# Optimization experiments

Hardware: AMD Instinct MI355X
Metric: run time of the kernel (lower is better)

The kernel has to match this reference:

```python
import jax, jax.numpy as jnp
import numpy as np

N_U, N_P, E, E_LAB = 100000, 50000, 2000000, 500000
D_U, D_P, H = 64, 128, 64


def _seg_mean(feat, idx, n):
    # scatter-mean: sum per destination / clamp(count, 1)
    s = jax.ops.segment_sum(feat, idx, num_segments=n)
    c = jax.ops.segment_sum(jnp.ones((idx.shape[0],), feat.dtype), idx, num_segments=n)
    return s / jnp.maximum(c, 1.0)[:, None]


def setup_inputs() -> dict:
    key = jax.random.key(0)
    ks = jax.random.split(key, 16)
    inp = {
        'x_user': jax.random.normal(ks[0], (N_U, D_U), jnp.float32),
        'x_product': jax.random.normal(ks[1], (N_P, D_P), jnp.float32),
        'W1_buys_l': jax.random.normal(ks[2], (D_U, H), jnp.float32) * 0.05,
        'b1_buys': jnp.zeros((H,), jnp.float32),
        'W1_buys_r': jax.random.normal(ks[3], (D_P, H), jnp.float32) * 0.05,
        'W1_rev_l': jax.random.normal(ks[4], (D_P, H), jnp.float32) * 0.05,
        'b1_rev': jnp.zeros((H,), jnp.float32),
        'W1_rev_r': jax.random.normal(ks[5], (D_U, H), jnp.float32) * 0.05,
        'W2_buys_l': jax.random.normal(ks[6], (H, H), jnp.float32) * 0.05,
        'b2_buys': jnp.zeros((H,), jnp.float32),
        'W2_buys_r': jax.random.normal(ks[7], (H, H), jnp.float32) * 0.05,
        'W2_rev_l': jax.random.normal(ks[8], (H, H), jnp.float32) * 0.05,
        'b2_rev': jnp.zeros((H,), jnp.float32),
        'W2_rev_r': jax.random.normal(ks[9], (H, H), jnp.float32) * 0.05,
        'edge_src': jax.random.randint(ks[10], (E,), 0, N_U, jnp.int32),
        'edge_dst': jax.random.randint(ks[11], (E,), 0, N_P, jnp.int32),
        'lab_u': jax.random.randint(ks[12], (E_LAB,), 0, N_U, jnp.int32),
        'lab_p': jax.random.randint(ks[13], (E_LAB,), 0, N_P, jnp.int32),
    }
    return inp


def reference(x_user, x_product, W1_buys_l, b1_buys, W1_buys_r, W1_rev_l, b1_rev, W1_rev_r,
              W2_buys_l, b2_buys, W2_buys_r, W2_rev_l, b2_rev, W2_rev_r,
              edge_src, edge_dst, lab_u, lab_p):
    # SAGEConv (mean aggr): out_dst = mean_agg(x_src) @ W_l + b + x_dst @ W_r
    def sage(x_src, x_dst, src, dst, n_dst, Wl, b, Wr):
        agg = _seg_mean(x_src[src], dst, n_dst)
        return agg @ Wl + b + x_dst @ Wr

    n_u, n_p = x_user.shape[0], x_product.shape[0]
    # layer 1 (per edge type, hetero) + relu
    h_p = jax.nn.relu(sage(x_user, x_product, edge_src, edge_dst, n_p, W1_buys_l, b1_buys, W1_buys_r))
    h_u = jax.nn.relu(sage(x_product, x_user, edge_dst, edge_src, n_u, W1_rev_l, b1_rev, W1_rev_r))
    # layer 2
    h_p2 = sage(h_u, h_p, edge_src, edge_dst, n_p, W2_buys_l, b2_buys, W2_buys_r)
    h_u2 = sage(h_p, h_u, edge_dst, edge_src, n_u, W2_rev_l, b2_rev, W2_rev_r)
    # classifier: per-label-edge dot product
    return jnp.sum(h_u2[lab_u] * h_p2[lab_p], axis=-1)
```

## Files before the change

### kernel.cpp

```cpp
#include <hip/hip_runtime.h>


using u16 = unsigned short;
using u32 = unsigned int;

__device__ __forceinline__ u16 bf16r(float f) {
    u32 b = __float_as_uint(f);
    b += 0x7fffu + ((b >> 16) & 1u);
    return (u16)(b >> 16);
}
__device__ __forceinline__ float bflo(u32 u) { return __uint_as_float(u << 16); }
__device__ __forceinline__ float bfhi(u32 u) { return __uint_as_float(u & 0xffff0000u); }

#define BSH 8
#define MAXB 512
#define CHUNK 4096
#define RPT 16

__global__ __launch_bounds__(256) void k_histA(const int* __restrict__ esrc,
                                               const int* __restrict__ edst,
                                               int* __restrict__ bcntP,
                                               int* __restrict__ bcntU,
                                               int NBP, int NBU, int E) {
    __shared__ int hP[MAXB];
    __shared__ int hU[MAXB];
    int tid = threadIdx.x;
    for (int i = tid; i < MAXB; i += 256) { hP[i] = 0; hU[i] = 0; }
    __syncthreads();
    int E4 = E >> 2;
    const int4* s4 = (const int4*)esrc;
    const int4* d4 = (const int4*)edst;
    int stride = gridDim.x * 256;
    for (int i = blockIdx.x * 256 + tid; i < E4; i += stride) {
        int4 s = s4[i], d = d4[i];
        atomicAdd(&hU[s.x >> BSH], 1); atomicAdd(&hU[s.y >> BSH], 1);
        atomicAdd(&hU[s.z >> BSH], 1); atomicAdd(&hU[s.w >> BSH], 1);
        atomicAdd(&hP[d.x >> BSH], 1); atomicAdd(&hP[d.y >> BSH], 1);
        atomicAdd(&hP[d.z >> BSH], 1); atomicAdd(&hP[d.w >> BSH], 1);
    }
    if (blockIdx.x == 0 && tid < (E & 3)) {
        int e = E4 * 4 + tid;
        atomicAdd(&hU[esrc[e] >> BSH], 1);
        atomicAdd(&hP[edst[e] >> BSH], 1);
    }
    __syncthreads();
    for (int i = tid; i < NBP; i += 256) if (hP[i]) atomicAdd(&bcntP[i], hP[i]);
    for (int i = tid; i < NBU; i += 256) if (hU[i]) atomicAdd(&bcntU[i], hU[i]);
}

__global__ __launch_bounds__(256) void k_scanBuckets(const int* __restrict__ cntP,
                                                     int* __restrict__ basesP,
                                                     int* __restrict__ curP, int NBP,
                                                     const int* __restrict__ cntU,
                                                     int* __restrict__ basesU,
                                                     int* __restrict__ curU, int NBU) {
    const int* cnt; int* bases; int* cur; int NB;
    if (blockIdx.x == 0) { cnt = cntP; bases = basesP; cur = curP; NB = NBP; }
    else                 { cnt = cntU; bases = basesU; cur = curU; NB = NBU; }
    __shared__ int sA[MAXB];
    __shared__ int sB[MAXB];
    int tid = threadIdx.x;
    int v0 = (tid < NB) ? cnt[tid] : 0;
    int v1 = (tid + 256 < NB) ? cnt[tid + 256] : 0;
    sA[tid] = v0; sA[tid + 256] = v1;
    __syncthreads();
    int* src = sA; int* dst = sB;
    for (int off = 1; off < MAXB; off <<= 1) {
        dst[tid] = src[tid] + ((tid >= off) ? src[tid - off] : 0);
        int i2 = tid + 256;
        dst[i2] = src[i2] + ((i2 >= off) ? src[i2 - off] : 0);
        __syncthreads();
        int* t = src; src = dst; dst = t;
    }
    if (tid < NB)       { bases[tid] = src[tid] - v0;             cur[tid] = src[tid] - v0; }
    if (tid + 256 < NB) { bases[tid + 256] = src[tid + 256] - v1; cur[tid + 256] = src[tid + 256] - v1; }
    if (tid == 0) bases[NB] = src[MAXB - 1];
}

__global__ __launch_bounds__(256) void k_partition(const int* __restrict__ keys,
                                                   const int* __restrict__ payload,
                                                   int* __restrict__ cursor,
                                                   uint2* __restrict__ pairs,
                                                   int NB, int E) {
    __shared__ int hist[MAXB];
    __shared__ int sA[MAXB];
    __shared__ int sB[MAXB];
    __shared__ int bx[MAXB];
    __shared__ int gbase[MAXB];
    __shared__ uint2 prs[CHUNK];
    int tid = threadIdx.x;
    int i0 = blockIdx.x * CHUNK;
    int count = min(CHUNK, E - i0);
    for (int i = tid; i < MAXB; i += 256) hist[i] = 0;
    __syncthreads();
    int keyr[RPT], payr[RPT], rankr[RPT];
#pragma unroll
    for (int r = 0; r < RPT; ++r) {
        int idx = r * 256 + tid;
        if (idx < count) {
            int k = keys[i0 + idx];
            keyr[r] = k;
            payr[r] = payload[i0 + idx];
            rankr[r] = atomicAdd(&hist[k >> BSH], 1);
        } else keyr[r] = -1;
    }
    __syncthreads();
    sA[tid] = hist[tid]; sA[tid + 256] = hist[tid + 256];
    __syncthreads();
    int* src = sA; int* dst = sB;
    for (int off = 1; off < MAXB; off <<= 1) {
        dst[tid] = src[tid] + ((tid >= off) ? src[tid - off] : 0);
        int i2 = tid + 256;
        dst[i2] = src[i2] + ((i2 >= off) ? src[i2 - off] : 0);
        __syncthreads();
        int* t = src; src = dst; dst = t;
    }
    bx[tid] = src[tid] - hist[tid];
    bx[tid + 256] = src[tid + 256] - hist[tid + 256];
    __syncthreads();
    for (int b = tid; b < NB; b += 256) {
        int c = hist[b];
        gbase[b] = c ? atomicAdd(&cursor[b], c) : 0;
    }
#pragma unroll
    for (int r = 0; r < RPT; ++r) {
        if (keyr[r] >= 0)
            prs[bx[keyr[r] >> BSH] + rankr[r]] = make_uint2((u32)keyr[r], (u32)payr[r]);
    }
    __syncthreads();
    for (int j = tid; j < count; j += 256) {
        uint2 pr = prs[j];
        int b = pr.x >> BSH;
        pairs[gbase[b] + (j - bx[b])] = pr;
    }
}

__global__ __launch_bounds__(256) void k_bucketFill(
    const uint2* __restrict__ pairsP, const int* __restrict__ basesP, int NBP,
    int* __restrict__ nbr_p, int* __restrict__ deg_p, int* __restrict__ ptr_p, int NP,
    const uint2* __restrict__ pairsU, const int* __restrict__ basesU, int NBU,
    int* __restrict__ nbr_u, int* __restrict__ deg_u, int* __restrict__ ptr_u, int NU) {
    const uint2* pairs; const int* bases; int* nbr; int* deg; int* ptr; int N; int bucket;
    if ((int)blockIdx.x < NBP) {
        pairs = pairsP; bases = basesP; nbr = nbr_p; deg = deg_p; ptr = ptr_p; N = NP;
        bucket = blockIdx.x;
    } else {
        pairs = pairsU; bases = basesU; nbr = nbr_u; deg = deg_u; ptr = ptr_u; N = NU;
        bucket = blockIdx.x - NBP;
    }
    int tid = threadIdx.x;
    int base = bases[bucket];
    int cnt = bases[bucket + 1] - base;
    __shared__ int h[256];
    __shared__ int s[256];
    __shared__ int cur[256];
    h[tid] = 0;
    __syncthreads();
    for (int j = tid; j < cnt; j += 256) atomicAdd(&h[pairs[base + j].x & 255], 1);
    __syncthreads();
    int d = h[tid];
    s[tid] = d;
    __syncthreads();
    for (int off = 1; off < 256; off <<= 1) {
        int v = (tid >= off) ? s[tid - off] : 0;
        __syncthreads();
        s[tid] += v;
        __syncthreads();
    }
    int excl = s[tid] - d;
    int node = bucket * 256 + tid;
    if (node < N) { deg[node] = d; ptr[node] = base + excl; }
    cur[tid] = excl;
    __syncthreads();
    for (int j = tid; j < cnt; j += 256) {
        uint2 pr = pairs[base + j];
        int pos = atomicAdd(&cur[pr.x & 255], 1);
        nbr[base + pos] = pr.y;
    }
}

__global__ __launch_bounds__(256) void k_cast8(const float* __restrict__ x,
                                               u16* __restrict__ y, int n8) {
    int i = blockIdx.x * 256 + threadIdx.x;
    if (i >= n8) return;
    const float4* x4 = (const float4*)x;
    float4 a = x4[i * 2], b = x4[i * 2 + 1];
    uint4 o;
    o.x = (u32)bf16r(a.x) | ((u32)bf16r(a.y) << 16);
    o.y = (u32)bf16r(a.z) | ((u32)bf16r(a.w) << 16);
    o.z = (u32)bf16r(b.x) | ((u32)bf16r(b.y) << 16);
    o.w = (u32)bf16r(b.z) | ((u32)bf16r(b.w) << 16);
    ((uint4*)y)[i] = o;
}

__global__ __launch_bounds__(256) void k_gather1(const u16* __restrict__ y,
                                                 const int* __restrict__ nbr,
                                                 const int* __restrict__ stp,
                                                 const int* __restrict__ degp,
                                                 float* __restrict__ agg, int N) {
    int n = (blockIdx.x * 256 + threadIdx.x) >> 6;
    int lane = threadIdx.x & 63;
    if (n >= N) return;
    const int q = lane >> 3, t = lane & 7;
    const int d = degp[n];
    int j = stp[n];
    const int end = j + d;
    float a0=0,a1=0,a2=0,a3=0,a4=0,a5=0,a6=0,a7=0;
    float b0=0,b1=0,b2=0,b3=0,b4=0,b5=0,b6=0,b7=0;
    for (; j + 16 <= end; j += 16) {
        int g0 = nbr[j + q], g1 = nbr[j + 8 + q];
        uint4 v0 = *(const uint4*)(y + g0 * 64 + t * 8);
        uint4 v1 = *(const uint4*)(y + g1 * 64 + t * 8);
        a0 += bflo(v0.x); a1 += bfhi(v0.x); a2 += bflo(v0.y); a3 += bfhi(v0.y);
        a4 += bflo(v0.z); a5 += bfhi(v0.z); a6 += bflo(v0.w); a7 += bfhi(v0.w);
        b0 += bflo(v1.x); b1 += bfhi(v1.x); b2 += bflo(v1.y); b3 += bfhi(v1.y);
        b4 += bflo(v1.z); b5 += bfhi(v1.z); b6 += bflo(v1.w); b7 += bfhi(v1.w);
    }
    for (; j + 8 <= end; j += 8) {
        int g0 = nbr[j + q];
        uint4 v0 = *(const uint4*)(y + g0 * 64 + t * 8);
        a0 += bflo(v0.x); a1 += bfhi(v0.x); a2 += bflo(v0.y); a3 += bfhi(v0.y);
        a4 += bflo(v0.z); a5 += bfhi(v0.z); a6 += bflo(v0.w); a7 += bfhi(v0.w);
    }
    if (j + q < end) {
        int g0 = nbr[j + q];
        uint4 v0 = *(const uint4*)(y + g0 * 64 + t * 8);
        a0 += bflo(v0.x); a1 += bfhi(v0.x); a2 += bflo(v0.y); a3 += bfhi(v0.y);
        a4 += bflo(v0.z); a5 += bfhi(v0.z); a6 += bflo(v0.w); a7 += bfhi(v0.w);
    }
    a0 += b0; a1 += b1; a2 += b2; a3 += b3; a4 += b4; a5 += b5; a6 += b6; a7 += b7;
#pragma unroll
    for (int m = 8; m < 64; m <<= 1) {
        a0 += __shfl_xor(a0, m, 64); a1 += __shfl_xor(a1, m, 64);
        a2 += __shfl_xor(a2, m, 64); a3 += __shfl_xor(a3, m, 64);
        a4 += __shfl_xor(a4, m, 64); a5 += __shfl_xor(a5, m, 64);
        a6 += __shfl_xor(a6, m, 64); a7 += __shfl_xor(a7, m, 64);
    }
    if (q == 0) {
        float dinv = 1.0f / (float)max(d, 1);
        float* dstp = agg + n * 64 + t * 8;
        *(float4*)dstp       = make_float4(a0 * dinv, a1 * dinv, a2 * dinv, a3 * dinv);
        *(float4*)(dstp + 4) = make_float4(a4 * dinv, a5 * dinv, a6 * dinv, a7 * dinv);
    }
}

#define FMA_ROW(ACC, O, W4) \
    ACC[0] += (O) * (W4).x; ACC[1] += (O) * (W4).y; \
    ACC[2] += (O) * (W4).z; ACC[3] += (O) * (W4).w;

template <int K, int ROWS, bool RELU, bool EMIT, bool PRE, bool BIAS, bool STORE>
__global__ __launch_bounds__(256) void k_ctile(const float* __restrict__ pre,
                                               const float* __restrict__ bias,
                                               const float* __restrict__ x,
                                               const float* __restrict__ W,
                                               float* __restrict__ h,
                                               u16* __restrict__ hbf, int N) {
    constexpr int RR = ROWS / 16;
    constexpr int STRIDE = K + 4;
    constexpr int KF4 = K / 4;
    __shared__ float Ws[K * 64];
    __shared__ float op[ROWS * STRIDE];
    const int tid = threadIdx.x;
    for (int i = tid; i < K * 16; i += 256)
        ((float4*)Ws)[i] = ((const float4*)W)[i];
    const int c4 = (tid & 15) * 4;
    const int rb = (tid >> 4) * RR;
    float bx_ = 0.f, by_ = 0.f, bz_ = 0.f, bw_ = 0.f;
    if (BIAS) {
        float4 b4 = *(const float4*)(bias + c4);
        bx_ = b4.x; by_ = b4.y; bz_ = b4.z; bw_ = b4.w;
    }
    const int ntiles = (N + ROWS - 1) / ROWS;
    for (int tile = blockIdx.x; tile < ntiles; tile += gridDim.x) {
        const int row0 = tile * ROWS;
        __syncthreads();
        for (int i = tid; i < ROWS * KF4; i += 256) {
            int r = i / KF4, k4 = (i % KF4) * 4;
            int row = row0 + r;
            float4 v = make_float4(0.f, 0.f, 0.f, 0.f);
            if (row < N) v = *(const float4*)(x + (size_t)row * K + k4);
            *(float4*)(op + r * STRIDE + k4) = v;
        }
        __syncthreads();
        float acc[RR][4];
#pragma unroll
        for (int i = 0; i < RR; ++i) {
            float px = 0.f, py = 0.f, pz = 0.f, pw = 0.f;
            if (PRE) {
                int row = row0 + rb + i;
                if (row < N) {
                    float4 p = *(const float4*)(pre + row * 64 + c4);
                    px = p.x; py = p.y; pz = p.z; pw = p.w;
                }
            }
            acc[i][0] = bx_ + px; acc[i][1] = by_ + py;
            acc[i][2] = bz_ + pz; acc[i][3] = bw_ + pw;
        }
        for (int kk = 0; kk < K; kk += 4) {
            float4 w0 = *(const float4*)(Ws + (kk + 0) * 64 + c4);
            float4 w1 = *(const float4*)(Ws + (kk + 1) * 64 + c4);
            float4 w2 = *(const float4*)(Ws + (kk + 2) * 64 + c4);
            float4 w3 = *(const float4*)(Ws + (kk + 3) * 64 + c4);
#pragma unroll
            for (int i = 0; i < RR; ++i) {
                float4 o = *(const float4*)(op + (rb + i) * STRIDE + kk);
                FMA_ROW(acc[i], o.x, w0);
                FMA_ROW(acc[i], o.y, w1);
                FMA_ROW(acc[i], o.z, w2);
                FMA_ROW(acc[i], o.w, w3);
            }
        }
#pragma unroll
        for (int i = 0; i < RR; ++i) {
            int row = row0 + rb + i;
            if (row >= N) continue;
            float v0 = acc[i][0], v1 = acc[i][1], v2 = acc[i][2], v3 = acc[i][3];
            if (RELU) {
                v0 = fmaxf(v0, 0.f); v1 = fmaxf(v1, 0.f);
                v2 = fmaxf(v2, 0.f); v3 = fmaxf(v3, 0.f);
            }
            if (STORE)
                *(float4*)(h + row * 64 + c4) = make_float4(v0, v1, v2, v3);
            if (EMIT) {
                uint2 o;
                o.x = (u32)bf16r(v0) | ((u32)bf16r(v1) << 16);
                o.y = (u32)bf16r(v2) | ((u32)bf16r(v3) << 16);
                *(uint2*)(hbf + row * 64 + c4) = o;
            }
        }
    }
}

__global__ __launch_bounds__(256) void k_classify4(const float* __restrict__ hu,
                                                   const float* __restrict__ hp,
                                                   const int* __restrict__ lu,
                                                   const int* __restrict__ lp,
                                                   float* __restrict__ out, int EL) {
    int w = (blockIdx.x * 256 + threadIdx.x) >> 6;
    int lane = threadIdx.x & 63;
    int q = lane >> 4, t = lane & 15;
    int e = w * 4 + q;
    float v = 0.f;
    if (e < EL) {
        int u = lu[e], p = lp[e];
        float4 a = *(const float4*)(hu + u * 64 + t * 4);
        float4 b = *(const float4*)(hp + p * 64 + t * 4);
        v = a.x * b.x + a.y * b.y + a.z * b.z + a.w * b.w;
    }
#pragma unroll
    for (int m = 1; m < 16; m <<= 1) v += __shfl_xor(v, m, 64);
    if (t == 0 && e < EL) out[e] = v;
}

extern "C" void kernel_launch(void* const* d_in, const int* in_sizes, int n_in,
                              void* d_out, int out_size, void* d_ws, size_t ws_size,
                              hipStream_t stream) {
    const float* x_user    = (const float*)d_in[0];
    const float* x_product = (const float*)d_in[1];
    const float* W1bl = (const float*)d_in[2];
    const float* b1b  = (const float*)d_in[3];
    const float* W1br = (const float*)d_in[4];
    const float* W1rl = (const float*)d_in[5];
    const float* b1r  = (const float*)d_in[6];
    const float* W1rr = (const float*)d_in[7];
    const float* W2bl = (const float*)d_in[8];
    const float* b2b  = (const float*)d_in[9];
    const float* W2br = (const float*)d_in[10];
    const float* W2rl = (const float*)d_in[11];
    const float* b2r  = (const float*)d_in[12];
    const float* W2rr = (const float*)d_in[13];
    const int* esrc = (const int*)d_in[14];
    const int* edst = (const int*)d_in[15];
    const int* lu   = (const int*)d_in[16];
    const int* lp   = (const int*)d_in[17];

    const int NU = in_sizes[0] / 64;
    const int NP = in_sizes[1] / 128;
    const int E  = in_sizes[14];
    const int EL = in_sizes[16];
    const int NBP = (NP + 255) >> BSH;
    const int NBU = (NU + 255) >> BSH;

    char* ws = (char*)d_ws;
    size_t off = 0;
    auto alloc = [&](size_t bytes) -> void* {
        void* p = ws + off;
        off += (bytes + 255) & ~(size_t)255;
        return p;
    };
    int*   deg_u  = (int*)alloc((size_t)NU * 4);
    int*   deg_p  = (int*)alloc((size_t)NP * 4);
    int*   ptr_u  = (int*)alloc((size_t)NU * 4);
    int*   ptr_p  = (int*)alloc((size_t)NP * 4);
    int*   bcntP  = (int*)alloc((size_t)MAXB * 4);
    int*   bcntU  = (int*)alloc((size_t)MAXB * 4);
    int*   basesP = (int*)alloc((size_t)(MAXB + 1) * 4);
    int*   basesU = (int*)alloc((size_t)(MAXB + 1) * 4);
    int*   curP   = (int*)alloc((size_t)MAXB * 4);
    int*   curU   = (int*)alloc((size_t)MAXB * 4);
    int*   nbr_u  = (int*)alloc((size_t)E * 4);
    int*   nbr_p  = (int*)alloc((size_t)E * 4);
    size_t aggBytes = (size_t)(NP + NU) * 64 * 4;
    size_t pairBytes = (size_t)E * 8 * 2;
    char* uni = (char*)alloc(aggBytes > pairBytes ? aggBytes : pairBytes);
    float* aggP   = (float*)uni;
    float* aggU   = (float*)(uni + (size_t)NP * 64 * 4);
    uint2* pairsP = (uint2*)uni;
    uint2* pairsU = (uint2*)(uni + (size_t)E * 8);
    u16*   bfA    = (u16*)alloc((size_t)NU * 64 * 2);
    u16*   bfB    = (u16*)alloc((size_t)NP * 64 * 2);
    float* h_p    = (float*)alloc((size_t)NP * 64 * 4);
    float* h_u    = (float*)alloc((size_t)NU * 64 * 4);

    hipMemsetAsync(bcntP, 0, (size_t)MAXB * 2 * 4, stream);
    k_histA<<<512, 256, 0, stream>>>(esrc, edst, bcntP, bcntU, NBP, NBU, E);
    k_scanBuckets<<<2, 256, 0, stream>>>(bcntP, basesP, curP, NBP, bcntU, basesU, curU, NBU);
    const int pblocks = (E + CHUNK - 1) / CHUNK;
    k_partition<<<pblocks, 256, 0, stream>>>(edst, esrc, curP, pairsP, NBP, E);
    k_partition<<<pblocks, 256, 0, stream>>>(esrc, edst, curU, pairsU, NBU, E);
    k_bucketFill<<<NBP + NBU, 256, 0, stream>>>(pairsP, basesP, NBP, nbr_p, deg_p, ptr_p, NP,
                                                pairsU, basesU, NBU, nbr_u, deg_u, ptr_u, NU);

    k_cast8<<<(NU * 64 / 8 + 255) / 256, 256, 0, stream>>>(x_user, bfA, NU * 64 / 8);
    {
        const int tiles = (NP + 31) / 32;
        k_ctile<128, 32, false, true, false, false, false><<<(tiles < 768 ? tiles : 768), 256, 0, stream>>>(
            nullptr, nullptr, x_product, W1rl, nullptr, bfB, NP);
    }

    const int tP64 = (NP + 63) / 64, tP32 = (NP + 31) / 32;
    const int tU64 = (NU + 63) / 64;
    auto cap = [](int t, int c) { return t < c ? t : c; };

    k_gather1<<<(NP + 3) / 4, 256, 0, stream>>>(bfA, nbr_p, ptr_p, deg_p, aggP, NP);
    k_gather1<<<(NU + 3) / 4, 256, 0, stream>>>(bfB, nbr_u, ptr_u, deg_u, aggU, NU);
    k_ctile<64, 64, false, false, false, true, true><<<cap(tP64, 1024), 256, 0, stream>>>(
        nullptr, b1b, aggP, W1bl, h_p, nullptr, NP);
    k_ctile<128, 32, true, true, true, false, true><<<cap(tP32, 768), 256, 0, stream>>>(
        h_p, nullptr, x_product, W1br, h_p, bfB, NP);
    k_ctile<64, 64, true, true, true, true, true><<<cap(tU64, 1024), 256, 0, stream>>>(
        aggU, b1r, x_user, W1rr, h_u, bfA, NU);

    k_gather1<<<(NP + 3) / 4, 256, 0, stream>>>(bfA, nbr_p, ptr_p, deg_p, aggP, NP);
    k_gather1<<<(NU + 3) / 4, 256, 0, stream>>>(bfB, nbr_u, ptr_u, deg_u, aggU, NU);
    k_ctile<64, 64, false, false, false, true, true><<<cap(tP64, 1024), 256, 0, stream>>>(
        nullptr, b2b, aggP, W2bl, aggP, nullptr, NP);
    k_ctile<64, 64, false, false, false, true, true><<<cap(tU64, 1024), 256, 0, stream>>>(
        nullptr, b2r, aggU, W2rl, aggU, nullptr, NU);
    k_ctile<64, 64, false, false, true, false, true><<<cap(tP64, 1024), 256, 0, stream>>>(
        aggP, nullptr, h_p, W2br, h_p, nullptr, NP);
    k_ctile<64, 64, false, false, true, false, true><<<cap(tU64, 1024), 256, 0, stream>>>(
        aggU, nullptr, h_u, W2rr, h_u, nullptr, NU);

    k_classify4<<<((EL + 3) / 4 + 3) / 4, 256, 0, stream>>>(h_u, h_p, lu, lp, (float*)d_out, EL);
}
```

Measured before the change: 549.7 us.

## Merge gather launches, deepen gather unroll, and classify from bf16 outputs

```diff
diff --git a/kernel.cpp b/kernel.cpp
--- a/kernel.cpp
+++ b/kernel.cpp
@@ -193,42 +193,59 @@
     ((uint4*)y)[i] = o;
 }
 
-__global__ __launch_bounds__(256) void k_gather1(const u16* __restrict__ y,
-                                                 const int* __restrict__ nbr,
-                                                 const int* __restrict__ stp,
-                                                 const int* __restrict__ degp,
-                                                 float* __restrict__ agg, int N) {
-    int n = (blockIdx.x * 256 + threadIdx.x) >> 6;
+#define ACC8(A0,A1,A2,A3,A4,A5,A6,A7,V) \
+    A0 += bflo((V).x); A1 += bfhi((V).x); A2 += bflo((V).y); A3 += bfhi((V).y); \
+    A4 += bflo((V).z); A5 += bfhi((V).z); A6 += bflo((V).w); A7 += bfhi((V).w);
+
+__global__ __launch_bounds__(256) void k_gather2(
+    const u16* __restrict__ yA, const int* __restrict__ nbrA, const int* __restrict__ stpA,
+    const int* __restrict__ degA, float* __restrict__ aggA, int NA,
+    const u16* __restrict__ yB, const int* __restrict__ nbrB, const int* __restrict__ stpB,
+    const int* __restrict__ degB, float* __restrict__ aggB, int NB) {
+    int w = (blockIdx.x * 256 + threadIdx.x) >> 6;
     int lane = threadIdx.x & 63;
-    if (n >= N) return;
+    if (w >= NA + NB) return;
+    const u16* y; const int* nbr; const int* stp; const int* deg; float* agg; int n;
+    if (w < NA) { y = yA; nbr = nbrA; stp = stpA; deg = degA; agg = aggA; n = w; }
+    else        { y = yB; nbr = nbrB; stp = stpB; deg = degB; agg = aggB; n = w - NA; }
     const int q = lane >> 3, t = lane & 7;
-    const int d = degp[n];
+    const int d = deg[n];
     int j = stp[n];
     const int end = j + d;
     float a0=0,a1=0,a2=0,a3=0,a4=0,a5=0,a6=0,a7=0;
     float b0=0,b1=0,b2=0,b3=0,b4=0,b5=0,b6=0,b7=0;
+    float c0=0,c1=0,c2=0,c3=0,c4=0,c5=0,c6=0,c7=0;
+    float e0=0,e1=0,e2=0,e3=0,e4=0,e5=0,e6=0,e7=0;
+    for (; j + 32 <= end; j += 32) {
+        int g0 = nbr[j + q], g1 = nbr[j + 8 + q], g2 = nbr[j + 16 + q], g3 = nbr[j + 24 + q];
+        uint4 v0 = *(const uint4*)(y + g0 * 64 + t * 8);
+        uint4 v1 = *(const uint4*)(y + g1 * 64 + t * 8);
+        uint4 v2 = *(const uint4*)(y + g2 * 64 + t * 8);
+        uint4 v3 = *(const uint4*)(y + g3 * 64 + t * 8);
+        ACC8(a0,a1,a2,a3,a4,a5,a6,a7,v0);
+        ACC8(b0,b1,b2,b3,b4,b5,b6,b7,v1);
+        ACC8(c0,c1,c2,c3,c4,c5,c6,c7,v2);
+        ACC8(e0,e1,e2,e3,e4,e5,e6,e7,v3);
+    }
     for (; j + 16 <= end; j += 16) {
         int g0 = nbr[j + q], g1 = nbr[j + 8 + q];
         uint4 v0 = *(const uint4*)(y + g0 * 64 + t * 8);
         uint4 v1 = *(const uint4*)(y + g1 * 64 + t * 8);
-        a0 += bflo(v0.x); a1 += bfhi(v0.x); a2 += bflo(v0.y); a3 += bfhi(v0.y);
-        a4 += bflo(v0.z); a5 += bfhi(v0.z); a6 += bflo(v0.w); a7 += bfhi(v0.w);
-        b0 += bflo(v1.x); b1 += bfhi(v1.x); b2 += bflo(v1.y); b3 += bfhi(v1.y);
-        b4 += bflo(v1.z); b5 += bfhi(v1.z); b6 += bflo(v1.w); b7 += bfhi(v1.w);
+        ACC8(a0,a1,a2,a3,a4,a5,a6,a7,v0);
+        ACC8(b0,b1,b2,b3,b4,b5,b6,b7,v1);
     }
     for (; j + 8 <= end; j += 8) {
         int g0 = nbr[j + q];
         uint4 v0 = *(const uint4*)(y + g0 * 64 + t * 8);
-        a0 += bflo(v0.x); a1 += bfhi(v0.x); a2 += bflo(v0.y); a3 += bfhi(v0.y);
-        a4 += bflo(v0.z); a5 += bfhi(v0.z); a6 += bflo(v0.w); a7 += bfhi(v0.w);
+        ACC8(a0,a1,a2,a3,a4,a5,a6,a7,v0);
     }
     if (j + q < end) {
         int g0 = nbr[j + q];
         uint4 v0 = *(const uint4*)(y + g0 * 64 + t * 8);
-        a0 += bflo(v0.x); a1 += bfhi(v0.x); a2 += bflo(v0.y); a3 += bfhi(v0.y);
-        a4 += bflo(v0.z); a5 += bfhi(v0.z); a6 += bflo(v0.w); a7 += bfhi(v0.w);
-    }
-    a0 += b0; a1 += b1; a2 += b2; a3 += b3; a4 += b4; a5 += b5; a6 += b6; a7 += b7;
+        ACC8(a0,a1,a2,a3,a4,a5,a6,a7,v0);
+    }
+    a0 += b0 + c0 + e0; a1 += b1 + c1 + e1; a2 += b2 + c2 + e2; a3 += b3 + c3 + e3;
+    a4 += b4 + c4 + e4; a5 += b5 + c5 + e5; a6 += b6 + c6 + e6; a7 += b7 + c7 + e7;
 #pragma unroll
     for (int m = 8; m < 64; m <<= 1) {
         a0 += __shfl_xor(a0, m, 64); a1 += __shfl_xor(a1, m, 64);
@@ -289,7 +306,7 @@
             if (PRE) {
                 int row = row0 + rb + i;
                 if (row < N) {
-                    float4 p = *(const float4*)(pre + row * 64 + c4);
+                    float4 p = *(const float4*)(pre + (size_t)row * 64 + c4);
                     px = p.x; py = p.y; pz = p.z; pw = p.w;
                 }
             }
@@ -331,11 +348,11 @@
     }
 }
 
-__global__ __launch_bounds__(256) void k_classify4(const float* __restrict__ hu,
-                                                   const float* __restrict__ hp,
-                                                   const int* __restrict__ lu,
-                                                   const int* __restrict__ lp,
-                                                   float* __restrict__ out, int EL) {
+__global__ __launch_bounds__(256) void k_classify4b(const u16* __restrict__ hu,
+                                                    const u16* __restrict__ hp,
+                                                    const int* __restrict__ lu,
+                                                    const int* __restrict__ lp,
+                                                    float* __restrict__ out, int EL) {
     int w = (blockIdx.x * 256 + threadIdx.x) >> 6;
     int lane = threadIdx.x & 63;
     int q = lane >> 4, t = lane & 15;
@@ -343,9 +360,10 @@
     float v = 0.f;
     if (e < EL) {
         int u = lu[e], p = lp[e];
-        float4 a = *(const float4*)(hu + u * 64 + t * 4);
-        float4 b = *(const float4*)(hp + p * 64 + t * 4);
-        v = a.x * b.x + a.y * b.y + a.z * b.z + a.w * b.w;
+        uint2 a = *(const uint2*)(hu + u * 64 + t * 4);
+        uint2 b = *(const uint2*)(hp + p * 64 + t * 4);
+        v = bflo(a.x) * bflo(b.x) + bfhi(a.x) * bfhi(b.x)
+          + bflo(a.y) * bflo(b.y) + bfhi(a.y) * bfhi(b.y);
     }
 #pragma unroll
     for (int m = 1; m < 16; m <<= 1) v += __shfl_xor(v, m, 64);
@@ -424,7 +442,8 @@
     k_cast8<<<(NU * 64 / 8 + 255) / 256, 256, 0, stream>>>(x_user, bfA, NU * 64 / 8);
     {
         const int tiles = (NP + 31) / 32;
-        k_ctile<128, 32, false, true, false, false, false><<<(tiles < 768 ? tiles : 768), 256, 0, stream>>>(
+        k_ctile<128, 32, false, true, false, false, false>
+            <<<(tiles < 768 ? tiles : 768), 256, 0, stream>>>(
             nullptr, nullptr, x_product, W1rl, nullptr, bfB, NP);
     }
 
@@ -432,8 +451,8 @@
     const int tU64 = (NU + 63) / 64;
     auto cap = [](int t, int c) { return t < c ? t : c; };
 
-    k_gather1<<<(NP + 3) / 4, 256, 0, stream>>>(bfA, nbr_p, ptr_p, deg_p, aggP, NP);
-    k_gather1<<<(NU + 3) / 4, 256, 0, stream>>>(bfB, nbr_u, ptr_u, deg_u, aggU, NU);
+    k_gather2<<<(NP + NU + 3) / 4, 256, 0, stream>>>(bfA, nbr_p, ptr_p, deg_p, aggP, NP,
+                                                     bfB, nbr_u, ptr_u, deg_u, aggU, NU);
     k_ctile<64, 64, false, false, false, true, true><<<cap(tP64, 1024), 256, 0, stream>>>(
         nullptr, b1b, aggP, W1bl, h_p, nullptr, NP);
     k_ctile<128, 32, true, true, true, false, true><<<cap(tP32, 768), 256, 0, stream>>>(
@@ -441,16 +460,16 @@
     k_ctile<64, 64, true, true, true, true, true><<<cap(tU64, 1024), 256, 0, stream>>>(
         aggU, b1r, x_user, W1rr, h_u, bfA, NU);
 
-    k_gather1<<<(NP + 3) / 4, 256, 0, stream>>>(bfA, nbr_p, ptr_p, deg_p, aggP, NP);
-    k_gather1<<<(NU + 3) / 4, 256, 0, stream>>>(bfB, nbr_u, ptr_u, deg_u, aggU, NU);
+    k_gather2<<<(NP + NU + 3) / 4, 256, 0, stream>>>(bfA, nbr_p, ptr_p, deg_p, aggP, NP,
+                                                     bfB, nbr_u, ptr_u, deg_u, aggU, NU);
     k_ctile<64, 64, false, false, false, true, true><<<cap(tP64, 1024), 256, 0, stream>>>(
         nullptr, b2b, aggP, W2bl, aggP, nullptr, NP);
     k_ctile<64, 64, false, false, false, true, true><<<cap(tU64, 1024), 256, 0, stream>>>(
         nullptr, b2r, aggU, W2rl, aggU, nullptr, NU);
-    k_ctile<64, 64, false, false, true, false, true><<<cap(tP64, 1024), 256, 0, stream>>>(
-        aggP, nullptr, h_p, W2br, h_p, nullptr, NP);
-    k_ctile<64, 64, false, false, true, false, true><<<cap(tU64, 1024), 256, 0, stream>>>(
-        aggU, nullptr, h_u, W2rr, h_u, nullptr, NU);
-
-    k_classify4<<<((EL + 3) / 4 + 3) / 4, 256, 0, stream>>>(h_u, h_p, lu, lp, (float*)d_out, EL);
-}
+    k_ctile<64, 64, false, true, true, false, false><<<cap(tP64, 1024), 256, 0, stream>>>(
+        aggP, nullptr, h_p, W2br, nullptr, bfB, NP);
+    k_ctile<64, 64, false, true, true, false, false><<<cap(tU64, 1024), 256, 0, stream>>>(
+        aggU, nullptr, h_u, W2rr, nullptr, bfA, NU);
+
+    k_classify4b<<<((EL + 3) / 4 + 3) / 4, 256, 0, stream>>>(bfA, bfB, lu, lp, (float*)d_out, EL);
+}
```

Result: slower. 605.5 us (+10.2%).
